# Kernel optimization log

Measured on AMD Instinct MI355X. Metric: run time of the kernel, lower is better.

## Reference

```python
import jax, jax.numpy as jnp
import numpy as np

N, H, D, G = 8192, 512, 256, 64
TAU, LAM, ALPHA, BETA = 0.5, 0.5, 1.0, 1.0
EPS_G, EPS_L = 1e-6, 1e-5


def setup_inputs() -> dict:
    key = jax.random.key(0)
    ks = jax.random.split(key, 8)
    za = jax.random.normal(ks[0], (N, H), dtype=jnp.float32)
    zb = jax.random.normal(ks[1], (N, H), dtype=jnp.float32)
    pos = jax.random.uniform(ks[2], (N, N), dtype=jnp.float32)
    batch = (jnp.arange(N, dtype=jnp.int32) * G) // N  # sorted, covers all G groups
    s_h = np.sqrt(2.0 / H).astype(np.float32)  # kaiming fan_in relu
    W1 = jax.random.normal(ks[3], (H, H), dtype=jnp.float32) * s_h
    b1 = jnp.zeros((H,), dtype=jnp.float32)
    W2 = jax.random.normal(ks[4], (H, H), dtype=jnp.float32) * s_h
    b2 = jnp.zeros((H,), dtype=jnp.float32)
    W3 = jax.random.normal(ks[5], (H, D), dtype=jnp.float32) * s_h
    b3 = jnp.zeros((D,), dtype=jnp.float32)
    a1 = jnp.full((1,), 0.5, dtype=jnp.float32)
    g1 = jnp.ones((H,), dtype=jnp.float32)
    be1 = jnp.zeros((H,), dtype=jnp.float32)
    a2 = jnp.full((1,), 0.5, dtype=jnp.float32)
    g2 = jnp.ones((H,), dtype=jnp.float32)
    be2 = jnp.zeros((H,), dtype=jnp.float32)
    return {"za": za, "zb": zb, "pos": pos, "batch": batch,
            "W1": W1, "b1": b1, "a1": a1, "g1": g1, "be1": be1,
            "W2": W2, "b2": b2, "a2": a2, "g2": g2, "be2": be2,
            "W3": W3, "b3": b3}


def _project(z, W1, b1, a1, g1, be1, W2, b2, a2, g2, be2, W3, b3):
    h = z @ W1 + b1
    h = jnp.tanh(a1 * h) * g1 + be1  # DyT
    h = h @ W2 + b2
    h = jnp.tanh(a2 * h) * g2 + be2  # DyT
    p = h @ W3 + b3
    return p * jax.nn.sigmoid(p)  # z1_proj * sigmoid(z1_proj)


def reference(za, zb, pos, batch, W1, b1, a1, g1, be1, W2, b2, a2, g2, be2, W3, b3):
    za_p = _project(za, W1, b1, a1, g1, be1, W2, b2, a2, g2, be2, W3, b3)
    zb_p = _project(zb, W1, b1, a1, g1, be1, W2, b2, a2, g2, be2, W3, b3)

    # exp(cosine / tau): same matrix used by global_contrast (sim) and local_contrast
    na = jnp.linalg.norm(za_p, axis=-1, keepdims=True)  # [N,1]
    nb = jnp.linalg.norm(zb_p, axis=-1, keepdims=True)  # [N,1]
    m = jnp.exp((za_p @ zb_p.T) / (na * nb.T) / TAU)    # [N,N]

    # global contrast
    a2b = m / (jnp.sum(m, axis=1, keepdims=True) + EPS_G)
    lori_a = -jnp.mean(jnp.log(jnp.sum(a2b * pos, axis=-1)))
    b2a = m.T
    b2a = b2a / (jnp.sum(b2a, axis=1, keepdims=True) + EPS_G)
    lori_b = -jnp.mean(jnp.log(jnp.sum(b2a * pos, axis=-1)))
    global_loss = LAM * lori_a + (1.0 - LAM) * lori_b

    # local contrast: per-group sums via one-hot matmul (replaces O(G^2) mask loop)
    pos_sim = jnp.diagonal(m)                              # [N]
    pos_sim_graph = jax.ops.segment_sum(pos_sim, batch, num_segments=G)  # [G]
    hot = jax.nn.one_hot(batch, G, dtype=m.dtype)          # [N,G]
    batch_sim = hot.T @ m @ hot                            # [G,G]
    graph_sim = jnp.diagonal(batch_sim)
    neg0 = jnp.sum(batch_sim, axis=0) - graph_sim
    neg1 = jnp.sum(batch_sim, axis=1) - graph_sim
    loss0 = jnp.mean(jnp.log(pos_sim_graph / (neg0 + EPS_L)))
    loss1 = jnp.mean(jnp.log(pos_sim_graph / (neg1 + EPS_L)))
    inter_loss = (loss0 + loss1) / 2.0
    inner_loss = -jnp.mean(jnp.log(pos_sim_graph / (graph_sim - pos_sim_graph + EPS_L)))
    local_loss = ALPHA * inter_loss + BETA * inner_loss

    total_loss = global_loss + local_loss
    return total_loss, jnp.concatenate((za_p, zb_p), axis=1)
```

## Files before the change

kernel.cpp:

```cpp
#include <hip/hip_runtime.h>
#include <hip/hip_bf16.h>
#include <cstdint>
#include <cstddef>


typedef __bf16 bf16;
typedef __bf16 bf16x4 __attribute__((ext_vector_type(4)));
typedef __bf16 bf16x8 __attribute__((ext_vector_type(8)));
typedef float  f32x4  __attribute__((ext_vector_type(4)));

#define NROWS 8192
#define HDIM  512
#define DDIM  256
#define GGRP  64
#define INV_TAU 2.0f

__device__ __forceinline__ void async_ld16(const void* g, void* l) {
    __builtin_amdgcn_global_load_lds(
        (__attribute__((address_space(1))) void*)(g),
        (__attribute__((address_space(3))) void*)(l), 16, 0, 0);
}

__device__ __forceinline__ void mfma_tile_128(
    const bf16* __restrict__ A, const bf16* __restrict__ Bt, int K,
    int row0, int col0, bf16* ldsA, bf16* ldsB, f32x4 acc[4][4], int tid)
{
    const int lane = tid & 63;
    const int wave = tid >> 6;
    const int wrow = (wave >> 1) * 64;
    const int wcol = (wave & 1) * 64;
    const int lrow = lane & 15;
    const int lk8  = (lane >> 4) * 8;

    const int sr = tid >> 2;
    const int sc = (tid & 3) * 8;
    const bf16* gA0 = A  + (size_t)(row0 + sr) * K + sc;
    const bf16* gA1 = gA0 + (size_t)64 * K;
    const bf16* gB0 = Bt + (size_t)(col0 + sr) * K + sc;
    const bf16* gB1 = gB0 + (size_t)64 * K;
    bf16* dA0 = ldsA + (wave * 64) * 8;
    bf16* dA1 = ldsA + (256 + wave * 64) * 8;
    bf16* dB0 = ldsB + (wave * 64) * 8;
    bf16* dB1 = ldsB + (256 + wave * 64) * 8;

#pragma unroll
    for (int i = 0; i < 4; i++)
#pragma unroll
        for (int j = 0; j < 4; j++) acc[i][j] = (f32x4){0.f, 0.f, 0.f, 0.f};

    for (int k0 = 0; k0 < K; k0 += 32) {
        async_ld16(gA0, dA0); async_ld16(gA1, dA1);
        async_ld16(gB0, dB0); async_ld16(gB1, dB1);
        gA0 += 32; gA1 += 32; gB0 += 32; gB1 += 32;
        __syncthreads();

        bf16x8 af[4], bfr[4];
#pragma unroll
        for (int fi = 0; fi < 4; fi++)
            af[fi] = *(const bf16x8*)(ldsA + (wrow + fi * 16 + lrow) * 32 + lk8);
#pragma unroll
        for (int fj = 0; fj < 4; fj++)
            bfr[fj] = *(const bf16x8*)(ldsB + (wcol + fj * 16 + lrow) * 32 + lk8);
#pragma unroll
        for (int fi = 0; fi < 4; fi++)
#pragma unroll
            for (int fj = 0; fj < 4; fj++)
                acc[fi][fj] = __builtin_amdgcn_mfma_f32_16x16x32_bf16(
                    af[fi], bfr[fj], acc[fi][fj], 0, 0, 0);
        __syncthreads();
    }
}

__global__ __launch_bounds__(256) void gemm_dyt(
    const bf16* __restrict__ A, const bf16* __restrict__ Bt, bf16* __restrict__ C,
    int K, int N,
    const float* __restrict__ bias, const float* __restrict__ alph,
    const float* __restrict__ gam, const float* __restrict__ bet)
{
    __shared__ __align__(16) bf16 ldsA[128 * 32];
    __shared__ __align__(16) bf16 ldsB[128 * 32];
    f32x4 acc[4][4];
    const int row0 = blockIdx.y * 128, col0 = blockIdx.x * 128;
    mfma_tile_128(A, Bt, K, row0, col0, ldsA, ldsB, acc, threadIdx.x);

    const int lane = threadIdx.x & 63, wave = threadIdx.x >> 6;
    const int wrow = (wave >> 1) * 64, wcol = (wave & 1) * 64;
    const int lcol = lane & 15, lrg = (lane >> 4) * 4;
    const float a = alph[0];
#pragma unroll
    for (int fi = 0; fi < 4; fi++) {
        const int rbase = row0 + wrow + fi * 16 + lrg;
#pragma unroll
        for (int fj = 0; fj < 4; fj++) {
            const int cg = col0 + wcol + fj * 16 + lcol;
            const float bcol = bias[cg], gcol = gam[cg], becol = bet[cg];
#pragma unroll
            for (int r = 0; r < 4; r++) {
                float x = acc[fi][fj][r] + bcol;
                float y = tanhf(a * x) * gcol + becol;
                C[(size_t)(rbase + r) * N + cg] = (bf16)y;
            }
        }
    }
}

__global__ __launch_bounds__(256) void gemm_silu(
    const bf16* __restrict__ A, const bf16* __restrict__ Bt,
    bf16* __restrict__ P16, float* __restrict__ out1, float* __restrict__ n2,
    const float* __restrict__ bias)
{
    __shared__ __align__(16) bf16 ldsA[128 * 32];
    __shared__ __align__(16) bf16 ldsB[128 * 32];
    f32x4 acc[4][4];
    const int row0 = blockIdx.y * 128, col0 = blockIdx.x * 128;
    mfma_tile_128(A, Bt, 512, row0, col0, ldsA, ldsB, acc, threadIdx.x);

    const int lane = threadIdx.x & 63, wave = threadIdx.x >> 6;
    const int wrow = (wave >> 1) * 64, wcol = (wave & 1) * 64;
    const int lcol = lane & 15, lrg = (lane >> 4) * 4;

    float nacc[4][4];
#pragma unroll
    for (int i = 0; i < 4; i++)
#pragma unroll
        for (int r = 0; r < 4; r++) nacc[i][r] = 0.f;

#pragma unroll
    for (int fi = 0; fi < 4; fi++) {
        const int rbase = row0 + wrow + fi * 16 + lrg;
#pragma unroll
        for (int fj = 0; fj < 4; fj++) {
            const int cg = col0 + wcol + fj * 16 + lcol;
            const float bcol = bias[cg];
#pragma unroll
            for (int r = 0; r < 4; r++) {
                const int rg = rbase + r;
                float x = acc[fi][fj][r] + bcol;
                float y = x / (1.f + __expf(-x));
                P16[(size_t)rg * 256 + cg] = (bf16)y;
                size_t oidx = (rg < NROWS) ? ((size_t)rg * 512 + cg)
                                           : ((size_t)(rg - NROWS) * 512 + 256 + cg);
                out1[oidx] = y;
                nacc[fi][r] += y * y;
            }
        }
    }
#pragma unroll
    for (int fi = 0; fi < 4; fi++)
#pragma unroll
        for (int r = 0; r < 4; r++) {
            float v = nacc[fi][r];
            v += __shfl_xor(v, 1); v += __shfl_xor(v, 2);
            v += __shfl_xor(v, 4); v += __shfl_xor(v, 8);
            if (lcol == 0)
                atomicAdd(&n2[row0 + wrow + fi * 16 + lrg + r], v);
        }
}

__global__ __launch_bounds__(512, 2) void sim_fused(
    const bf16* __restrict__ PA, const bf16* __restrict__ PB,
    const float* __restrict__ rnA, const float* __restrict__ rnB,
    const float* __restrict__ pos,
    float* __restrict__ rowsum, float* __restrict__ colsum,
    float* __restrict__ s_a, float* __restrict__ s_b,
    float* __restrict__ bsim, float* __restrict__ psg)
{
    __shared__ __align__(16) bf16 lds[2][2][128 * 32];
    const int half = threadIdx.x >> 8;
    const int tid  = threadIdx.x & 255;
    const int I = blockIdx.y, J = blockIdx.x;
    const int row0 = I * 128, col0 = J * 128;

    const bf16* Aop = half ? PB : PA;
    const bf16* Bop = half ? PA : PB;
    const float* rnR = half ? rnB : rnA;
    const float* rnC = half ? rnA : rnB;
    float* outR = half ? colsum : rowsum;
    float* outS = half ? s_b : s_a;

    const int lane = tid & 63, wave = tid >> 6;
    const int wrow = (wave >> 1) * 64, wcol = (wave & 1) * 64;
    const int lcol = lane & 15, lrg = (lane >> 4) * 4;

    float pv[4][4][4];
#pragma unroll
    for (int fi = 0; fi < 4; fi++)
#pragma unroll
        for (int r = 0; r < 4; r++) {
            const float* prow = pos + (size_t)(row0 + wrow + fi * 16 + lrg + r) * NROWS
                                    + col0 + wcol + lcol;
#pragma unroll
            for (int fj = 0; fj < 4; fj++) pv[fi][fj][r] = prow[fj * 16];
        }

    f32x4 acc[4][4];
    mfma_tile_128(Aop, Bop, 256, row0, col0,
                  (bf16*)lds[half][0], (bf16*)lds[half][1], acc, tid);

    float racc[4][4], sacc[4][4];
#pragma unroll
    for (int i = 0; i < 4; i++)
#pragma unroll
        for (int r = 0; r < 4; r++) { racc[i][r] = 0.f; sacc[i][r] = 0.f; }
    float msum = 0.f;

#pragma unroll
    for (int fi = 0; fi < 4; fi++) {
        const int rbase = row0 + wrow + fi * 16 + lrg;
        float rna[4];
#pragma unroll
        for (int r = 0; r < 4; r++) rna[r] = rnR[rbase + r] * INV_TAU;
#pragma unroll
        for (int fj = 0; fj < 4; fj++) {
            const int cg = col0 + wcol + fj * 16 + lcol;
            const float rnc = rnC[cg];
#pragma unroll
            for (int r = 0; r < 4; r++) {
                float mval = __expf(acc[fi][fj][r] * rna[r] * rnc);
                racc[fi][r] += mval;
                sacc[fi][r] += mval * pv[fi][fj][r];
                if (half == 0) {
                    msum += mval;
                    if (I == J && (rbase + r) == cg)
                        atomicAdd(&psg[I], mval);
                }
            }
        }
    }
#pragma unroll
    for (int fi = 0; fi < 4; fi++)
#pragma unroll
        for (int r = 0; r < 4; r++) {
            float rv = racc[fi][r], sv = sacc[fi][r];
            rv += __shfl_xor(rv, 1); rv += __shfl_xor(rv, 2);
            rv += __shfl_xor(rv, 4); rv += __shfl_xor(rv, 8);
            sv += __shfl_xor(sv, 1); sv += __shfl_xor(sv, 2);
            sv += __shfl_xor(sv, 4); sv += __shfl_xor(sv, 8);
            if (lcol == 0) {
                const int rg = row0 + wrow + fi * 16 + lrg + r;
                atomicAdd(&outR[rg], rv);
                atomicAdd(&outS[rg], sv);
            }
        }
    if (half == 0) {
        msum += __shfl_xor(msum, 1);  msum += __shfl_xor(msum, 2);
        msum += __shfl_xor(msum, 4);  msum += __shfl_xor(msum, 8);
        msum += __shfl_xor(msum, 16); msum += __shfl_xor(msum, 32);
        if (lane == 0) atomicAdd(&bsim[I * GGRP + J], msum);
    }
}

__global__ void cast4_kernel(const float4* __restrict__ x, bf16x4* __restrict__ y, int n4)
{
    int i = blockIdx.x * blockDim.x + threadIdx.x;
    if (i < n4) {
        float4 v = x[i];
        bf16x4 o;
        o[0] = (bf16)v.x; o[1] = (bf16)v.y; o[2] = (bf16)v.z; o[3] = (bf16)v.w;
        y[i] = o;
    }
}

__global__ void transpose_cast(const float* __restrict__ W, bf16* __restrict__ Wt,
                               int R, int C)
{
    __shared__ float tile[32][33];
    const int c0 = blockIdx.x * 32, r0 = blockIdx.y * 32;
    const int tx = threadIdx.x, ty = threadIdx.y;
    for (int i = ty; i < 32; i += 8)
        tile[i][tx] = W[(size_t)(r0 + i) * C + c0 + tx];
    __syncthreads();
    for (int i = ty; i < 32; i += 8)
        Wt[(size_t)(c0 + i) * R + r0 + tx] = (bf16)tile[tx][i];
}

__global__ void rsqrt_kernel(const float* __restrict__ x, float* __restrict__ y, int n)
{
    int i = blockIdx.x * blockDim.x + threadIdx.x;
    if (i < n) y[i] = rsqrtf(fmaxf(x[i], 1e-30f));
}

__global__ __launch_bounds__(256) void loss_rows(
    const float* __restrict__ sa, const float* __restrict__ rowsum,
    const float* __restrict__ sb, const float* __restrict__ colsum,
    float* __restrict__ gsum)
{
    __shared__ float red[8];
    const int i = blockIdx.x * 256 + threadIdx.x;
    float la = __logf(sa[i] / (rowsum[i] + 1e-6f));
    float lb = __logf(sb[i] / (colsum[i] + 1e-6f));
    for (int m = 1; m < 64; m <<= 1) { la += __shfl_xor(la, m); lb += __shfl_xor(lb, m); }
    const int w = threadIdx.x >> 6;
    if ((threadIdx.x & 63) == 0) { red[w] = la; red[4 + w] = lb; }
    __syncthreads();
    if (threadIdx.x == 0)  atomicAdd(&gsum[0], red[0] + red[1] + red[2] + red[3]);
    if (threadIdx.x == 64) atomicAdd(&gsum[1], red[4] + red[5] + red[6] + red[7]);
}

__global__ void loss_final(
    const float* __restrict__ bs, const float* __restrict__ psg,
    const float* __restrict__ gsum, float* __restrict__ out)
{
    const int t = threadIdx.x;
    float c0 = 0.f, c1 = 0.f;
    for (int a = 0; a < GGRP; a++) { c0 += bs[a * GGRP + t]; c1 += bs[t * GGRP + a]; }
    const float d = bs[t * (GGRP + 1)];
    const float p = psg[t];
    float l0  = __logf(p / (c0 - d + 1e-5f));
    float l1  = __logf(p / (c1 - d + 1e-5f));
    float lin = __logf(p / (d - p + 1e-5f));
    for (int m = 1; m < 64; m <<= 1) {
        l0 += __shfl_xor(l0, m); l1 += __shfl_xor(l1, m); lin += __shfl_xor(lin, m);
    }
    if (t == 0) {
        const float lori_a = -gsum[0] / (float)NROWS;
        const float lori_b = -gsum[1] / (float)NROWS;
        const float global_loss = 0.5f * (lori_a + lori_b);
        const float inter = 0.5f * (l0 + l1) / (float)GGRP;
        const float inner = -lin / (float)GGRP;
        out[0] = global_loss + inter + inner;
    }
}

extern "C" void kernel_launch(void* const* d_in, const int* in_sizes, int n_in,
                              void* d_out, int out_size, void* d_ws, size_t ws_size,
                              hipStream_t stream)
{
    const float* za  = (const float*)d_in[0];
    const float* zb  = (const float*)d_in[1];
    const float* pos = (const float*)d_in[2];
    const float* W1  = (const float*)d_in[4];
    const float* b1  = (const float*)d_in[5];
    const float* a1  = (const float*)d_in[6];
    const float* g1  = (const float*)d_in[7];
    const float* be1 = (const float*)d_in[8];
    const float* W2  = (const float*)d_in[9];
    const float* b2  = (const float*)d_in[10];
    const float* a2  = (const float*)d_in[11];
    const float* g2  = (const float*)d_in[12];
    const float* be2 = (const float*)d_in[13];
    const float* W3  = (const float*)d_in[14];
    const float* b3  = (const float*)d_in[15];
    float* out = (float*)d_out;

    char* ws = (char*)d_ws;
    float* rowsum = (float*)(ws);
    float* colsum = rowsum + 8192;
    float* s_a    = colsum + 8192;
    float* s_b    = s_a + 8192;
    float* n2     = s_b + 8192;
    float* bsim   = n2 + 16384;
    float* psg    = bsim + 4096;
    float* gsum   = psg + 64;
    const size_t accum_bytes = (size_t)(8192 * 4 + 16384 + 4096 + 64 + 2) * 4;

    float* rn  = (float*)(ws + 213504);
    bf16* Z16  = (bf16*)(ws + 213504 + 65536);
    bf16* h1   = Z16 + (size_t)16384 * 512;
    bf16* p16  = h1 + (size_t)16384 * 512;
    bf16* W1t  = p16 + (size_t)16384 * 256;
    bf16* W2t  = W1t + (size_t)512 * 512;
    bf16* W3t  = W2t + (size_t)512 * 512;

    hipMemsetAsync(d_ws, 0, accum_bytes, stream);

    const int n4 = NROWS * HDIM / 4;
    cast4_kernel<<<n4 / 256, 256, 0, stream>>>((const float4*)za, (bf16x4*)Z16, n4);
    cast4_kernel<<<n4 / 256, 256, 0, stream>>>((const float4*)zb,
                                               (bf16x4*)(Z16 + (size_t)NROWS * HDIM), n4);
    dim3 tb(32, 8);
    transpose_cast<<<dim3(16, 16), tb, 0, stream>>>(W1, W1t, 512, 512);
    transpose_cast<<<dim3(16, 16), tb, 0, stream>>>(W2, W2t, 512, 512);
    transpose_cast<<<dim3(8, 16),  tb, 0, stream>>>(W3, W3t, 512, 256);

    gemm_dyt<<<dim3(4, 128), 256, 0, stream>>>(Z16, W1t, h1, 512, 512, b1, a1, g1, be1);
    gemm_dyt<<<dim3(4, 128), 256, 0, stream>>>(h1, W2t, Z16 , 512, 512, b2, a2, g2, be2);
    gemm_silu<<<dim3(2, 128), 256, 0, stream>>>(Z16, W3t, p16, out + 1, n2, b3);
    rsqrt_kernel<<<16384 / 256, 256, 0, stream>>>(n2, rn, 16384);

    const bf16* pa = p16;
    const bf16* pb = p16 + (size_t)NROWS * DDIM;
    sim_fused<<<dim3(64, 64), 512, 0, stream>>>(pa, pb, rn, rn + NROWS, pos,
                                                rowsum, colsum, s_a, s_b, bsim, psg);

    loss_rows<<<32, 256, 0, stream>>>(s_a, rowsum, s_b, colsum, gsum);
    loss_final<<<1, 64, 0, stream>>>(bsim, psg, gsum, out);
}
```

Baseline: 904.3 us.

## Split fused similarity kernel into two passes with LDS-staged pos tiles

The single 512-thread kernel computed both the row-direction and column-direction tiles per block. It is replaced by a templated 256-thread kernel launched twice, once per direction. Each launch streams its 128x128 pos tile into LDS with async global-to-LDS loads alongside the inline bf16 operand loads, instead of strided per-lane register loads. This aims for better coalescing and less register pressure. The cost is that pos, which is large, is now read from memory twice across two launches rather than once per block, and the new K-loop is single-buffered with two barriers per step.

After: 863.2 us. -4.5%, faster.

```diff
diff --git a/kernel.cpp b/kernel.cpp
--- a/kernel.cpp
+++ b/kernel.cpp
@@ -157,46 +157,72 @@
         }
 }
 
-__global__ __launch_bounds__(512, 2) void sim_fused(
+template <int PASS1>
+__global__ __launch_bounds__(256, 2) void sim_pass(
     const bf16* __restrict__ PA, const bf16* __restrict__ PB,
     const float* __restrict__ rnA, const float* __restrict__ rnB,
     const float* __restrict__ pos,
-    float* __restrict__ rowsum, float* __restrict__ colsum,
-    float* __restrict__ s_a, float* __restrict__ s_b,
+    float* __restrict__ rsum, float* __restrict__ wsum,
     float* __restrict__ bsim, float* __restrict__ psg)
 {
-    __shared__ __align__(16) bf16 lds[2][2][128 * 32];
-    const int half = threadIdx.x >> 8;
-    const int tid  = threadIdx.x & 255;
+    __shared__ __align__(16) bf16  ldsA[128 * 32];
+    __shared__ __align__(16) bf16  ldsB[128 * 32];
+    __shared__ __align__(16) float ldsP[128 * 128];
+
+    const int tid  = threadIdx.x;
+    const int lane = tid & 63, wave = tid >> 6;
+    const int wrow = (wave >> 1) * 64, wcol = (wave & 1) * 64;
+    const int lrow = lane & 15, lk8 = (lane >> 4) * 8;
     const int I = blockIdx.y, J = blockIdx.x;
     const int row0 = I * 128, col0 = J * 128;
 
-    const bf16* Aop = half ? PB : PA;
-    const bf16* Bop = half ? PA : PB;
-    const float* rnR = half ? rnB : rnA;
-    const float* rnC = half ? rnA : rnB;
-    float* outR = half ? colsum : rowsum;
-    float* outS = half ? s_b : s_a;
-
-    const int lane = tid & 63, wave = tid >> 6;
-    const int wrow = (wave >> 1) * 64, wcol = (wave & 1) * 64;
+    const int sr = tid >> 2, sc = (tid & 3) * 8;
+    const bf16* gA0 = PA + (size_t)(row0 + sr) * DDIM + sc;
+    const bf16* gA1 = gA0 + (size_t)64 * DDIM;
+    const bf16* gB0 = PB + (size_t)(col0 + sr) * DDIM + sc;
+    const bf16* gB1 = gB0 + (size_t)64 * DDIM;
+    bf16* dA0 = ldsA + (wave * 64) * 8;
+    bf16* dA1 = ldsA + (256 + wave * 64) * 8;
+    bf16* dB0 = ldsB + (wave * 64) * 8;
+    bf16* dB1 = ldsB + (256 + wave * 64) * 8;
+
+    const int pr0 = tid >> 5;
+    const int pc0 = (tid & 31) * 4;
+    const float* gP0 = pos + (size_t)(row0 + pr0) * NROWS + col0 + pc0;
+    const float* gP1 = gP0 + (size_t)8 * NROWS;
+    float* dP = ldsP + wave * 256;
+
+    f32x4 acc[4][4];
+#pragma unroll
+    for (int i = 0; i < 4; i++)
+#pragma unroll
+        for (int j = 0; j < 4; j++) acc[i][j] = (f32x4){0.f, 0.f, 0.f, 0.f};
+
+    for (int it = 0; it < 8; ++it) {
+        async_ld16(gA0, dA0); async_ld16(gA1, dA1);
+        async_ld16(gB0, dB0); async_ld16(gB1, dB1);
+        async_ld16(gP0, dP);  async_ld16(gP1, dP + 1024);
+        gA0 += 32; gA1 += 32; gB0 += 32; gB1 += 32;
+        gP0 += (size_t)16 * NROWS; gP1 += (size_t)16 * NROWS; dP += 2048;
+        __syncthreads();
+
+        bf16x8 af[4], bfr[4];
+#pragma unroll
+        for (int fi = 0; fi < 4; fi++)
+            af[fi] = *(const bf16x8*)(ldsA + (wrow + fi * 16 + lrow) * 32 + lk8);
+#pragma unroll
+        for (int fj = 0; fj < 4; fj++)
+            bfr[fj] = *(const bf16x8*)(ldsB + (wcol + fj * 16 + lrow) * 32 + lk8);
+#pragma unroll
+        for (int fi = 0; fi < 4; fi++)
+#pragma unroll
+            for (int fj = 0; fj < 4; fj++)
+                acc[fi][fj] = __builtin_amdgcn_mfma_f32_16x16x32_bf16(
+                    af[fi], bfr[fj], acc[fi][fj], 0, 0, 0);
+        __syncthreads();
+    }
+
     const int lcol = lane & 15, lrg = (lane >> 4) * 4;
-
-    float pv[4][4][4];
-#pragma unroll
-    for (int fi = 0; fi < 4; fi++)
-#pragma unroll
-        for (int r = 0; r < 4; r++) {
-            const float* prow = pos + (size_t)(row0 + wrow + fi * 16 + lrg + r) * NROWS
-                                    + col0 + wcol + lcol;
-#pragma unroll
-            for (int fj = 0; fj < 4; fj++) pv[fi][fj][r] = prow[fj * 16];
-        }
-
-    f32x4 acc[4][4];
-    mfma_tile_128(Aop, Bop, 256, row0, col0,
-                  (bf16*)lds[half][0], (bf16*)lds[half][1], acc, tid);
-
     float racc[4][4], sacc[4][4];
 #pragma unroll
     for (int i = 0; i < 4; i++)
@@ -206,20 +232,23 @@
 
 #pragma unroll
     for (int fi = 0; fi < 4; fi++) {
-        const int rbase = row0 + wrow + fi * 16 + lrg;
+        const int rl = wrow + fi * 16 + lrg;
+        const int rbase = row0 + rl;
         float rna[4];
 #pragma unroll
-        for (int r = 0; r < 4; r++) rna[r] = rnR[rbase + r] * INV_TAU;
+        for (int r = 0; r < 4; r++) rna[r] = rnA[rbase + r] * INV_TAU;
 #pragma unroll
         for (int fj = 0; fj < 4; fj++) {
-            const int cg = col0 + wcol + fj * 16 + lcol;
-            const float rnc = rnC[cg];
+            const int cl = wcol + fj * 16 + lcol;
+            const int cg = col0 + cl;
+            const float rnb = rnB[cg];
 #pragma unroll
             for (int r = 0; r < 4; r++) {
-                float mval = __expf(acc[fi][fj][r] * rna[r] * rnc);
+                float mval = __expf(acc[fi][fj][r] * rna[r] * rnb);
+                float pv = ldsP[(rl + r) * 128 + cl];
                 racc[fi][r] += mval;
-                sacc[fi][r] += mval * pv[fi][fj][r];
-                if (half == 0) {
+                sacc[fi][r] += mval * pv;
+                if (PASS1) {
                     msum += mval;
                     if (I == J && (rbase + r) == cg)
                         atomicAdd(&psg[I], mval);
@@ -238,11 +267,11 @@
             sv += __shfl_xor(sv, 4); sv += __shfl_xor(sv, 8);
             if (lcol == 0) {
                 const int rg = row0 + wrow + fi * 16 + lrg + r;
-                atomicAdd(&outR[rg], rv);
-                atomicAdd(&outS[rg], sv);
+                atomicAdd(&rsum[rg], rv);
+                atomicAdd(&wsum[rg], sv);
             }
         }
-    if (half == 0) {
+    if (PASS1) {
         msum += __shfl_xor(msum, 1);  msum += __shfl_xor(msum, 2);
         msum += __shfl_xor(msum, 4);  msum += __shfl_xor(msum, 8);
         msum += __shfl_xor(msum, 16); msum += __shfl_xor(msum, 32);
@@ -380,8 +409,10 @@
 
     const bf16* pa = p16;
     const bf16* pb = p16 + (size_t)NROWS * DDIM;
-    sim_fused<<<dim3(64, 64), 512, 0, stream>>>(pa, pb, rn, rn + NROWS, pos,
-                                                rowsum, colsum, s_a, s_b, bsim, psg);
+    sim_pass<1><<<dim3(64, 64), 256, 0, stream>>>(pa, pb, rn, rn + NROWS, pos,
+                                                  rowsum, s_a, bsim, psg);
+    sim_pass<0><<<dim3(64, 64), 256, 0, stream>>>(pb, pa, rn + NROWS, rn, pos,
+                                                  colsum, s_b, nullptr, nullptr);
 
     loss_rows<<<32, 256, 0, stream>>>(s_a, rowsum, s_b, colsum, gsum);
     loss_final<<<1, 64, 0, stream>>>(bsim, psg, gsum, out);
```
